# Performance work log

Measured on AMD Instinct MI355X. Metric: run time of the kernel, lower is better.

The kernel has to match this reference:

```python
import jax, jax.numpy as jnp
import numpy as np

TOKENS = 8192      # batch*seq flattened
D_IN = 2048        # in_features (power of 2 for Hadamard)
D_OUT = 8192       # out_features

try:
    FP8 = jnp.float8_e4m3fn
except AttributeError:
    FP8 = None


def fwht(x):
    """Normalized fast Walsh-Hadamard transform over last dim (power of 2)."""
    orig_shape = x.shape
    n = orig_shape[-1]
    x = x.reshape(-1, n)
    h = 1
    while h < n:
        x = x.reshape(-1, n // (2 * h), 2, h)
        a = x[..., 0, :]
        b = x[..., 1, :]
        x = jnp.stack([a + b, a - b], axis=-2).reshape(-1, n)
        h *= 2
    return (x * (1.0 / np.sqrt(n))).reshape(orig_shape)


def setup_inputs() -> dict:
    key = jax.random.key(0)
    kx, kw, kb = jax.random.split(key, 3)
    x = jax.random.normal(kx, (TOKENS, D_IN), dtype=jnp.float32)
    # Weight is stored in fp8 e4m3 (quantized in the Hadamard domain);
    # we materialize its dequantized fp32 values for the reference math.
    w = jax.random.normal(kw, (D_OUT, D_IN), dtype=jnp.float32) * 0.02
    if FP8 is not None:
        w = w.astype(FP8).astype(jnp.float32)  # simulate fp8 storage round-trip
    b = jax.random.normal(kb, (D_OUT,), dtype=jnp.float32) * 0.01
    return {"x": x, "weight": w, "bias": b}


def reference(x, weight, bias):
    # use_hadamard=True: rotate activations into the Hadamard domain
    # (weight was quantized in that domain), then fp8-dequant GEMM + bias.
    x_h = fwht(x)                               # [T, D_IN]
    out = jnp.einsum('td,od->to', x_h, weight)  # [T, D_OUT]
    return out + bias[None, :]
```

## Files before the change

kernel.cpp:

```cpp
#include <hip/hip_runtime.h>
#include <hip/hip_bf16.h>
#include <stdint.h>

#define TOKENS 8192
#define D_IN   2048
#define D_OUT  8192
#define BK     64
#define NT     (D_IN / BK)

typedef __attribute__((ext_vector_type(8))) short short8;
typedef __attribute__((ext_vector_type(4))) float floatx4;

__device__ __forceinline__ void async_copy16(const void* g, void* l) {
    __builtin_amdgcn_global_load_lds((const __attribute__((address_space(1))) void*)g,
                                     (__attribute__((address_space(3))) void*)l,
                                     16, 0, 0);
}

__device__ __forceinline__ void fwht8(float* e) {
#pragma unroll
    for (int s = 1; s < 8; s <<= 1) {
#pragma unroll
        for (int j = 0; j < 8; ++j) {
            if ((j & s) == 0) {
                float a = e[j], b = e[j | s];
                e[j]     = a + b;
                e[j | s] = a - b;
            }
        }
    }
}

__global__ __launch_bounds__(256) void fwht_kernel(const float* __restrict__ x,
                                                   __hip_bfloat16* __restrict__ xh) {
    __shared__ float row[D_IN];
    const int r = blockIdx.x;
    const int t = threadIdx.x;
    const float* xr = x + (size_t)r * D_IN;

    float e[8];
#pragma unroll
    for (int j = 0; j < 8; ++j) e[j] = xr[t + 256 * j];
    fwht8(e);
#pragma unroll
    for (int j = 0; j < 8; ++j) row[t + 256 * j] = e[j];
    __syncthreads();

    float f[8];
#pragma unroll
    for (int j = 0; j < 8; ++j) f[j] = row[8 * t + j];
    fwht8(f);
#pragma unroll
    for (int m = 1; m <= 16; m <<= 1) {
#pragma unroll
        for (int j = 0; j < 8; ++j) {
            float v = __shfl_xor(f[j], m, 64);
            f[j] = (t & m) ? (v - f[j]) : (f[j] + v);
        }
    }

    const float scale = 0.02209708691207961f;
    __hip_bfloat16 ob[8];
#pragma unroll
    for (int j = 0; j < 8; ++j) ob[j] = __float2bfloat16(f[j] * scale);
    __hip_bfloat16* orow = xh + (size_t)r * D_IN + 8 * t;
    *reinterpret_cast<int4*>(orow) = *reinterpret_cast<int4*>(ob);
}

__global__ __launch_bounds__(256) void wconv_kernel(const float* __restrict__ w,
                                                    __hip_bfloat16* __restrict__ wb) {
    const size_t i = ((size_t)blockIdx.x * 256 + threadIdx.x) * 8;
    float4 a = *reinterpret_cast<const float4*>(w + i);
    float4 b = *reinterpret_cast<const float4*>(w + i + 4);
    __hip_bfloat16 ob[8];
    ob[0] = __float2bfloat16(a.x); ob[1] = __float2bfloat16(a.y);
    ob[2] = __float2bfloat16(a.z); ob[3] = __float2bfloat16(a.w);
    ob[4] = __float2bfloat16(b.x); ob[5] = __float2bfloat16(b.y);
    ob[6] = __float2bfloat16(b.z); ob[7] = __float2bfloat16(b.w);
    *reinterpret_cast<int4*>(wb + i) = *reinterpret_cast<int4*>(ob);
}

__global__ __launch_bounds__(512, 2) void gemm_kernel(const __hip_bfloat16* __restrict__ A,
                                                      const __hip_bfloat16* __restrict__ B,
                                                      const float* __restrict__ bias,
                                                      float* __restrict__ C) {
    extern __shared__ float4 smem_f4[];
    __hip_bfloat16* sA = (__hip_bfloat16*)smem_f4;
    __hip_bfloat16* sB = sA + 2 * 16384;

    const int tid    = threadIdx.x;
    const int wave   = tid >> 6;
    const int lane   = tid & 63;
    const int lane16 = lane & 15;
    const int lgrp   = lane >> 4;

    const int bid = blockIdx.x;
    const int xcd = bid & 7;
    const int loc = bid >> 3;
    const int rnd = loc >> 5;
    const int pos = loc & 31;
    const int bm  = xcd * 4 + (pos >> 3);
    const int bn  = rnd * 8 + (pos & 7);

    const int wm = wave >> 2;
    const int wn = wave & 3;

    const int srow = lane >> 3;
    const int scc8 = ((lane & 7) ^ srow) * 8;
    const int r0   = wave * 16 + srow;
    const __hip_bfloat16* gAst = A + (size_t)(bm * 256) * D_IN + scc8;
    const __hip_bfloat16* gBst = B + (size_t)(bn * 256) * D_IN + scc8;

    auto stageA = [&](int kt, int h) {
        const __hip_bfloat16* g = gAst + (size_t)(h * 128 + r0) * D_IN + kt * BK;
        __hip_bfloat16* l = sA + (kt & 1) * 16384 + h * 8192 + wave * 1024;
        async_copy16(g, l);
        async_copy16(g + (size_t)8 * D_IN, l + 512);
    };
    auto stageB = [&](int kt, int h) {
        const __hip_bfloat16* g = gBst + (size_t)(h * 128 + r0) * D_IN + kt * BK;
        __hip_bfloat16* l = sB + (kt & 1) * 16384 + h * 8192 + wave * 1024;
        async_copy16(g, l);
        async_copy16(g + (size_t)8 * D_IN, l + 512);
    };

    const int sw   = lane16 & 7;
    const int cK0  = ((0 + lgrp) ^ sw) * 8;
    const int cK1  = ((4 + lgrp) ^ sw) * 8;
    const int arow = wm * 128 + lane16;
    const int brow = wn * 64  + lane16;

    floatx4 acc[8][4];
#pragma unroll
    for (int m = 0; m < 8; ++m)
#pragma unroll
        for (int n = 0; n < 4; ++n) acc[m][n] = 0;

    stageA(0, 0); stageA(0, 1);
    stageB(0, 0); stageB(0, 1);
    stageA(1, 0); stageA(1, 1);
    __builtin_amdgcn_sched_barrier(0);
    asm volatile("s_waitcnt vmcnt(4)");
    __builtin_amdgcn_s_barrier();
    __builtin_amdgcn_sched_barrier(0);

    short8 af[8][2];
    short8 bf[4][2];

#pragma unroll 2
    for (int kt = 0; kt < NT; ++kt) {
        const __hip_bfloat16* curA = sA + ((kt & 1) << 14);
        const __hip_bfloat16* curB = sB + ((kt & 1) << 14);

#pragma unroll
        for (int m = 0; m < 4; ++m) {
            const __hip_bfloat16* p = curA + (arow + m * 16) * 64;
            af[m][0] = *reinterpret_cast<const short8*>(p + cK0);
            af[m][1] = *reinterpret_cast<const short8*>(p + cK1);
        }
#pragma unroll
        for (int n = 0; n < 2; ++n) {
            const __hip_bfloat16* p = curB + (brow + n * 16) * 64;
            bf[n][0] = *reinterpret_cast<const short8*>(p + cK0);
            bf[n][1] = *reinterpret_cast<const short8*>(p + cK1);
        }
        if (kt + 1 < NT) stageB(kt + 1, 0);
        __builtin_amdgcn_s_barrier();
        asm volatile("s_waitcnt lgkmcnt(0)");
        __builtin_amdgcn_sched_barrier(0);
        __builtin_amdgcn_s_setprio(1);
#pragma unroll
        for (int m = 0; m < 4; ++m)
#pragma unroll
            for (int n = 0; n < 2; ++n) {
                acc[m][n] = __builtin_amdgcn_mfma_f32_16x16x32_bf16(af[m][0], bf[n][0], acc[m][n], 0, 0, 0);
                acc[m][n] = __builtin_amdgcn_mfma_f32_16x16x32_bf16(af[m][1], bf[n][1], acc[m][n], 0, 0, 0);
            }
        __builtin_amdgcn_s_setprio(0);
        __builtin_amdgcn_s_barrier();

#pragma unroll
        for (int m = 4; m < 8; ++m) {
            const __hip_bfloat16* p = curA + (arow + m * 16) * 64;
            af[m][0] = *reinterpret_cast<const short8*>(p + cK0);
            af[m][1] = *reinterpret_cast<const short8*>(p + cK1);
        }
        if (kt + 1 < NT) stageB(kt + 1, 1);
        __builtin_amdgcn_s_barrier();
        asm volatile("s_waitcnt lgkmcnt(0)");
        __builtin_amdgcn_sched_barrier(0);
        __builtin_amdgcn_s_setprio(1);
#pragma unroll
        for (int m = 4; m < 8; ++m)
#pragma unroll
            for (int n = 0; n < 2; ++n) {
                acc[m][n] = __builtin_amdgcn_mfma_f32_16x16x32_bf16(af[m][0], bf[n][0], acc[m][n], 0, 0, 0);
                acc[m][n] = __builtin_amdgcn_mfma_f32_16x16x32_bf16(af[m][1], bf[n][1], acc[m][n], 0, 0, 0);
            }
        __builtin_amdgcn_s_setprio(0);
        __builtin_amdgcn_s_barrier();

#pragma unroll
        for (int n = 2; n < 4; ++n) {
            const __hip_bfloat16* p = curB + (brow + n * 16) * 64;
            bf[n][0] = *reinterpret_cast<const short8*>(p + cK0);
            bf[n][1] = *reinterpret_cast<const short8*>(p + cK1);
        }
        if (kt + 2 < NT) stageA(kt + 2, 0);
        __builtin_amdgcn_s_barrier();
        asm volatile("s_waitcnt lgkmcnt(0)");
        __builtin_amdgcn_sched_barrier(0);
        __builtin_amdgcn_s_setprio(1);
#pragma unroll
        for (int m = 0; m < 4; ++m)
#pragma unroll
            for (int n = 2; n < 4; ++n) {
                acc[m][n] = __builtin_amdgcn_mfma_f32_16x16x32_bf16(af[m][0], bf[n][0], acc[m][n], 0, 0, 0);
                acc[m][n] = __builtin_amdgcn_mfma_f32_16x16x32_bf16(af[m][1], bf[n][1], acc[m][n], 0, 0, 0);
            }
        __builtin_amdgcn_s_setprio(0);
        __builtin_amdgcn_s_barrier();

        if (kt + 2 < NT) stageA(kt + 2, 1);
        __builtin_amdgcn_s_barrier();
        asm volatile("s_waitcnt lgkmcnt(0)");
        __builtin_amdgcn_sched_barrier(0);
        __builtin_amdgcn_s_setprio(1);
#pragma unroll
        for (int m = 4; m < 8; ++m)
#pragma unroll
            for (int n = 2; n < 4; ++n) {
                acc[m][n] = __builtin_amdgcn_mfma_f32_16x16x32_bf16(af[m][0], bf[n][0], acc[m][n], 0, 0, 0);
                acc[m][n] = __builtin_amdgcn_mfma_f32_16x16x32_bf16(af[m][1], bf[n][1], acc[m][n], 0, 0, 0);
            }
        __builtin_amdgcn_s_setprio(0);
        __builtin_amdgcn_sched_barrier(0);
        if (kt + 2 < NT) {
            asm volatile("s_waitcnt vmcnt(4)");
        } else {
            asm volatile("s_waitcnt vmcnt(0)");
        }
        __builtin_amdgcn_s_barrier();
        __builtin_amdgcn_sched_barrier(0);
    }

    float bv[4];
#pragma unroll
    for (int n = 0; n < 4; ++n) bv[n] = bias[bn * 256 + wn * 64 + n * 16 + lane16];

#pragma unroll
    for (int m = 0; m < 8; ++m) {
        const int rbase = bm * 256 + wm * 128 + m * 16 + lgrp * 4;
#pragma unroll
        for (int n = 0; n < 4; ++n) {
            const int col = bn * 256 + wn * 64 + n * 16 + lane16;
#pragma unroll
            for (int r = 0; r < 4; ++r) {
                C[(size_t)(rbase + r) * D_OUT + col] = acc[m][n][r] + bv[n];
            }
        }
    }
}

extern "C" void kernel_launch(void* const* d_in, const int* in_sizes, int n_in,
                              void* d_out, int out_size, void* d_ws, size_t ws_size,
                              hipStream_t stream) {
    const float* x    = (const float*)d_in[0];
    const float* w    = (const float*)d_in[1];
    const float* bias = (const float*)d_in[2];
    float* out = (float*)d_out;

    __hip_bfloat16* xh = (__hip_bfloat16*)d_ws;
    __hip_bfloat16* wb = xh + (size_t)TOKENS * D_IN;

    static bool attr_set = false;
    if (!attr_set) {
        (void)hipFuncSetAttribute((const void*)gemm_kernel,
                                  hipFuncAttributeMaxDynamicSharedMemorySize, 131072);
        attr_set = true;
    }

    fwht_kernel<<<TOKENS, 256, 0, stream>>>(x, xh);
    wconv_kernel<<<(D_OUT * D_IN / 8) / 256, 256, 0, stream>>>(w, wb);
    gemm_kernel<<<1024, 512, 131072, stream>>>(xh, wb, bias, out);
}
```

Baseline: 554.5 us.

## Prefetch next-tile LDS fragments during MFMA phases with partial lgkmcnt waits

Restructures the four-phase main loop of the bf16 MFMA GEMM so that A and B register fragments for the next K tile are read from LDS during the current tile's compute phases. The first fragments are preloaded before the loop. Waits are relaxed to partial lgkmcnt/vmcnt counts so LDS reads and global-to-LDS copies can overlap with MFMA work. The cost is more complex barrier and wait-count reasoning, with a risk of races or wrong counts if the staging order does not match.

```diff
diff --git a/kernel.cpp b/kernel.cpp
--- a/kernel.cpp
+++ b/kernel.cpp
@@ -146,38 +146,25 @@
 
     short8 af[8][2];
     short8 bf[4][2];
+#pragma unroll
+    for (int m = 0; m < 4; ++m) {
+        const __hip_bfloat16* p = sA + (arow + m * 16) * 64;
+        af[m][0] = *reinterpret_cast<const short8*>(p + cK0);
+        af[m][1] = *reinterpret_cast<const short8*>(p + cK1);
+    }
+#pragma unroll
+    for (int n = 0; n < 4; ++n) {
+        const __hip_bfloat16* p = sB + (brow + n * 16) * 64;
+        bf[n][0] = *reinterpret_cast<const short8*>(p + cK0);
+        bf[n][1] = *reinterpret_cast<const short8*>(p + cK1);
+    }
+    __builtin_amdgcn_sched_barrier(0);
 
 #pragma unroll 2
     for (int kt = 0; kt < NT; ++kt) {
         const __hip_bfloat16* curA = sA + ((kt & 1) << 14);
-        const __hip_bfloat16* curB = sB + ((kt & 1) << 14);
-
-#pragma unroll
-        for (int m = 0; m < 4; ++m) {
-            const __hip_bfloat16* p = curA + (arow + m * 16) * 64;
-            af[m][0] = *reinterpret_cast<const short8*>(p + cK0);
-            af[m][1] = *reinterpret_cast<const short8*>(p + cK1);
-        }
-#pragma unroll
-        for (int n = 0; n < 2; ++n) {
-            const __hip_bfloat16* p = curB + (brow + n * 16) * 64;
-            bf[n][0] = *reinterpret_cast<const short8*>(p + cK0);
-            bf[n][1] = *reinterpret_cast<const short8*>(p + cK1);
-        }
-        if (kt + 1 < NT) stageB(kt + 1, 0);
-        __builtin_amdgcn_s_barrier();
-        asm volatile("s_waitcnt lgkmcnt(0)");
-        __builtin_amdgcn_sched_barrier(0);
-        __builtin_amdgcn_s_setprio(1);
-#pragma unroll
-        for (int m = 0; m < 4; ++m)
-#pragma unroll
-            for (int n = 0; n < 2; ++n) {
-                acc[m][n] = __builtin_amdgcn_mfma_f32_16x16x32_bf16(af[m][0], bf[n][0], acc[m][n], 0, 0, 0);
-                acc[m][n] = __builtin_amdgcn_mfma_f32_16x16x32_bf16(af[m][1], bf[n][1], acc[m][n], 0, 0, 0);
-            }
-        __builtin_amdgcn_s_setprio(0);
-        __builtin_amdgcn_s_barrier();
+        const __hip_bfloat16* nxtA = sA + (((kt + 1) & 1) << 14);
+        const __hip_bfloat16* nxtB = sB + (((kt + 1) & 1) << 14);
 
 #pragma unroll
         for (int m = 4; m < 8; ++m) {
@@ -185,13 +172,14 @@
             af[m][0] = *reinterpret_cast<const short8*>(p + cK0);
             af[m][1] = *reinterpret_cast<const short8*>(p + cK1);
         }
-        if (kt + 1 < NT) stageB(kt + 1, 1);
-        __builtin_amdgcn_s_barrier();
-        asm volatile("s_waitcnt lgkmcnt(0)");
+        __builtin_amdgcn_sched_barrier(0);
+        if (kt + 1 < NT) stageB(kt + 1, 0);
+        __builtin_amdgcn_s_barrier();
+        asm volatile("s_waitcnt lgkmcnt(8)");
         __builtin_amdgcn_sched_barrier(0);
         __builtin_amdgcn_s_setprio(1);
 #pragma unroll
-        for (int m = 4; m < 8; ++m)
+        for (int m = 0; m < 4; ++m)
 #pragma unroll
             for (int n = 0; n < 2; ++n) {
                 acc[m][n] = __builtin_amdgcn_mfma_f32_16x16x32_bf16(af[m][0], bf[n][0], acc[m][n], 0, 0, 0);
@@ -199,14 +187,9 @@
             }
         __builtin_amdgcn_s_setprio(0);
         __builtin_amdgcn_s_barrier();
-
-#pragma unroll
-        for (int n = 2; n < 4; ++n) {
-            const __hip_bfloat16* p = curB + (brow + n * 16) * 64;
-            bf[n][0] = *reinterpret_cast<const short8*>(p + cK0);
-            bf[n][1] = *reinterpret_cast<const short8*>(p + cK1);
-        }
-        if (kt + 2 < NT) stageA(kt + 2, 0);
+        __builtin_amdgcn_sched_barrier(0);
+
+        if (kt + 1 < NT) stageB(kt + 1, 1);
         __builtin_amdgcn_s_barrier();
         asm volatile("s_waitcnt lgkmcnt(0)");
         __builtin_amdgcn_sched_barrier(0);
@@ -220,10 +203,27 @@
             }
         __builtin_amdgcn_s_setprio(0);
         __builtin_amdgcn_s_barrier();
-
-        if (kt + 2 < NT) stageA(kt + 2, 1);
-        __builtin_amdgcn_s_barrier();
-        asm volatile("s_waitcnt lgkmcnt(0)");
+        __builtin_amdgcn_sched_barrier(0);
+
+        if (kt + 2 < NT) {
+            stageA(kt + 2, 0);
+            __builtin_amdgcn_sched_barrier(0);
+            asm volatile("s_waitcnt vmcnt(6)");
+        } else if (kt + 1 < NT) {
+            asm volatile("s_waitcnt vmcnt(4)");
+        }
+        __builtin_amdgcn_s_barrier();
+        __builtin_amdgcn_sched_barrier(0);
+        if (kt + 1 < NT) {
+#pragma unroll
+            for (int m = 0; m < 4; ++m) {
+                const __hip_bfloat16* p = nxtA + (arow + m * 16) * 64;
+                af[m][0] = *reinterpret_cast<const short8*>(p + cK0);
+                af[m][1] = *reinterpret_cast<const short8*>(p + cK1);
+            }
+        }
+        __builtin_amdgcn_sched_barrier(0);
+        asm volatile("s_waitcnt lgkmcnt(8)");
         __builtin_amdgcn_sched_barrier(0);
         __builtin_amdgcn_s_setprio(1);
 #pragma unroll
@@ -234,12 +234,45 @@
                 acc[m][n] = __builtin_amdgcn_mfma_f32_16x16x32_bf16(af[m][1], bf[n][1], acc[m][n], 0, 0, 0);
             }
         __builtin_amdgcn_s_setprio(0);
-        __builtin_amdgcn_sched_barrier(0);
+        __builtin_amdgcn_s_barrier();
+        __builtin_amdgcn_sched_barrier(0);
+
         if (kt + 2 < NT) {
+            stageA(kt + 2, 1);
+            __builtin_amdgcn_sched_barrier(0);
             asm volatile("s_waitcnt vmcnt(4)");
         } else {
             asm volatile("s_waitcnt vmcnt(0)");
         }
+        __builtin_amdgcn_s_barrier();
+        __builtin_amdgcn_sched_barrier(0);
+        if (kt + 1 < NT) {
+#pragma unroll
+            for (int n = 2; n < 4; ++n) {
+                const __hip_bfloat16* p = nxtB + (brow + n * 16) * 64;
+                bf[n][0] = *reinterpret_cast<const short8*>(p + cK0);
+                bf[n][1] = *reinterpret_cast<const short8*>(p + cK1);
+            }
+        }
+        __builtin_amdgcn_sched_barrier(0);
+        __builtin_amdgcn_s_setprio(1);
+#pragma unroll
+        for (int m = 4; m < 8; ++m)
+#pragma unroll
+            for (int n = 0; n < 2; ++n) {
+                acc[m][n] = __builtin_amdgcn_mfma_f32_16x16x32_bf16(af[m][0], bf[n][0], acc[m][n], 0, 0, 0);
+                acc[m][n] = __builtin_amdgcn_mfma_f32_16x16x32_bf16(af[m][1], bf[n][1], acc[m][n], 0, 0, 0);
+            }
+        __builtin_amdgcn_s_setprio(0);
+        if (kt + 1 < NT) {
+#pragma unroll
+            for (int n = 0; n < 2; ++n) {
+                const __hip_bfloat16* p = nxtB + (brow + n * 16) * 64;
+                bf[n][0] = *reinterpret_cast<const short8*>(p + cK0);
+                bf[n][1] = *reinterpret_cast<const short8*>(p + cK1);
+            }
+        }
+        __builtin_amdgcn_sched_barrier(0);
         __builtin_amdgcn_s_barrier();
         __builtin_amdgcn_sched_barrier(0);
     }
```

New measurement: 633.1 us. 1.14x slower.
